# Kernel tuning notes

Measured on AMD Instinct MI355X. Metric: run time of the kernel, lower is better.

The kernel has to match this reference:

```python
import jax, jax.numpy as jnp
import numpy as np

B, P, T, R, A = 16384, 3, 2, 3, 3   # batch, n_players, teammates, rivals, action_dim
HID = [1024, 512]
ENC_OUT = 64
RIVAL_START = 9 * 9 + 12 * P       # 117, as in the torch module
NEG_SLOPE = 0.01                    # nn.LeakyReLU default


def _linpack(key, k, din, dout):
    # PyTorch nn.Linear default init: U(-1/sqrt(din), 1/sqrt(din))
    kw, kb = jax.random.split(key)
    bound = 1.0 / np.sqrt(din)
    W = jax.random.uniform(kw, (k, din, dout), jnp.float32, -bound, bound)
    b = jax.random.uniform(kb, (k, dout), jnp.float32, -bound, bound)
    return W, b


def setup_inputs() -> dict:
    key = jax.random.key(0)
    ks = jax.random.split(key, 16)
    obs = jax.random.normal(ks[0], (B, P, 144), jnp.float32)
    act = jax.random.normal(ks[1], (B, P, A), jnp.float32)
    # stacked per-segment encoder weights (grouped small GEMMs)
    Wp1, bp1 = _linpack(ks[2], 9, 2 + A, 32)
    Wp2, bp2 = _linpack(ks[3], 9, 32, ENC_OUT)
    Wt1, bt1 = _linpack(ks[4], T, 12, 32)
    Wt2, bt2 = _linpack(ks[5], T, 32, ENC_OUT)
    Wr1, br1 = _linpack(ks[6], R, 9, 32)
    Wr2, br2 = _linpack(ks[7], R, 32, ENC_OUT)
    # q head: [P*896] -> 1024 -> 512 -> P
    din = P * (9 + T + R) * ENC_OUT
    Wq1, bq1 = _linpack(ks[8], 1, din, HID[0]);  Wq1, bq1 = Wq1[0], bq1[0]
    Wq2, bq2 = _linpack(ks[9], 1, HID[0], HID[1]); Wq2, bq2 = Wq2[0], bq2[0]
    Wq3, bq3 = _linpack(ks[10], 1, HID[1], P);   Wq3, bq3 = Wq3[0], bq3[0]
    return dict(obs=obs, act=act,
                Wp1=Wp1, bp1=bp1, Wp2=Wp2, bp2=bp2,
                Wt1=Wt1, bt1=bt1, Wt2=Wt2, bt2=bt2,
                Wr1=Wr1, br1=br1, Wr2=Wr2, br2=br2,
                Wq1=Wq1, bq1=bq1, Wq2=Wq2, bq2=bq2, Wq3=Wq3, bq3=bq3)


def _enc2(x, W1, b1, W2, b2):
    # x: [B, P, K, din]; W1: [K, din, 32]; W2: [K, 32, 64] -> [B, P, K, 64]
    lrelu = lambda v: jax.nn.leaky_relu(v, NEG_SLOPE)
    h = lrelu(jnp.einsum('bpki,kio->bpko', x, W1) + b1)
    return lrelu(jnp.einsum('bpkh,kho->bpko', h, W2) + b2)


def reference(obs, act, Wp1, bp1, Wp2, bp2, Wt1, bt1, Wt2, bt2,
              Wr1, br1, Wr2, br2, Wq1, bq1, Wq2, bq2, Wq3, bq3):
    b = obs.shape[0]
    # prop segments: obs[:, :, 2i:2i+2] concat act  -> [B, P, 9, 2+A]
    x_prop = jnp.concatenate(
        [obs[:, :, :18].reshape(b, P, 9, 2),
         jnp.broadcast_to(act[:, :, None, :], (b, P, 9, A))], axis=-1)
    x_team = obs[:, :, 18:18 + 12 * T].reshape(b, P, T, 12)
    x_riv = obs[:, :, RIVAL_START:RIVAL_START + 9 * R].reshape(b, P, R, 9)
    ep = _enc2(x_prop, Wp1, bp1, Wp2, bp2)   # [B, P, 9, 64]
    et = _enc2(x_team, Wt1, bt1, Wt2, bt2)   # [B, P, T, 64]
    er = _enc2(x_riv, Wr1, br1, Wr2, br2)    # [B, P, R, 64]
    enc = jnp.concatenate([ep, et, er], axis=2).reshape(b, -1)  # [B, P*14*64]
    # q head: ReLU hidden activations, identity output
    h = jax.nn.relu(enc @ Wq1 + bq1)
    h = jax.nn.relu(h @ Wq2 + bq2)
    return h @ Wq3 + bq3                      # [B, P]
```

## Files before the change

kernel.cpp:

```cpp
#include <hip/hip_runtime.h>
#include <hip/hip_bf16.h>
#include <cstdint>

typedef __bf16 bf16x8 __attribute__((ext_vector_type(8)));
typedef float f32x4 __attribute__((ext_vector_type(4)));

__device__ __forceinline__ void gld16(const __bf16* g, __bf16* lds) {
    __builtin_amdgcn_global_load_lds(
        (__attribute__((address_space(1))) void*)(uintptr_t)g,
        (__attribute__((address_space(3))) void*)(uint32_t)(uintptr_t)lds,
        16, 0, 0);
}

__global__ __launch_bounds__(256) void prep_all(const float* __restrict__ Wq1, const float* __restrict__ Wq2,
                                                const float* __restrict__ Wp1, const float* __restrict__ bp1,
                                                const float* __restrict__ Wp2, const float* __restrict__ bp2,
                                                const float* __restrict__ Wt1, const float* __restrict__ bt1,
                                                const float* __restrict__ Wt2, const float* __restrict__ bt2,
                                                const float* __restrict__ Wr1, const float* __restrict__ br1,
                                                const float* __restrict__ Wr2, const float* __restrict__ br2,
                                                __bf16* __restrict__ w1t, __bf16* __restrict__ w2t,
                                                float* __restrict__ w1p, __bf16* __restrict__ w2e) {
    __shared__ float t[64][65];
    const int idx = blockIdx.x, tid = threadIdx.x;
    if (idx < 800) {
        const float* in; __bf16* out; int R, C, bx, by;
        if (idx < 672) { in = Wq1; out = w1t; R = 2688; C = 1024; bx = idx % 42; by = idx / 42; }
        else { const int i2 = idx - 672; in = Wq2; out = w2t; R = 1024; C = 512; bx = i2 % 16; by = i2 / 16; }
        const int r0 = bx * 64, c0 = by * 64;
#pragma unroll
        for (int i = 0; i < 16; i++) {
            int id2 = i * 256 + tid;
            int rr = id2 >> 6, cc = id2 & 63;
            t[rr][cc] = in[(size_t)(r0 + rr) * C + (c0 + cc)];
        }
        __syncthreads();
#pragma unroll
        for (int i = 0; i < 16; i++) {
            int id2 = i * 256 + tid;
            int rr = id2 >> 6, cc = id2 & 63;
            out[(size_t)(c0 + rr) * R + (r0 + cc)] = (__bf16)t[cc][rr];
        }
    } else {
        const int s = idx - 800;
        int ks, din, w1off;
        const float *W1, *B1, *W2, *B2;
        if (s < 9)      { ks = s;      din = 5;  w1off = s * 160;
                          W1 = Wp1; B1 = bp1; W2 = Wp2; B2 = bp2; }
        else if (s < 11){ ks = s - 9;  din = 12; w1off = 1440 + ks * 384;
                          W1 = Wt1; B1 = bt1; W2 = Wt2; B2 = bt2; }
        else            { ks = s - 11; din = 9;  w1off = 2208 + ks * 288;
                          W1 = Wr1; B1 = br1; W2 = Wr2; B2 = br2; }
        W1 += ks * din * 32; B1 += ks * 32; W2 += ks * 2048; B2 += ks * 64;
        for (int i = tid; i < din * 32; i += 256) w1p[w1off + i] = W1[i];
        if (tid < 32) w1p[3072 + s * 32 + tid] = B1[tid];
        if (tid < 64) w1p[3520 + s * 64 + tid] = B2[tid];
        for (int i = tid; i < 2048; i += 256) {
            const int o = i >> 5, k = i & 31;
            w2e[s * 2048 + i] = (__bf16)W2[k * 64 + o];
        }
    }
}

__global__ __launch_bounds__(256) void enc_fused(const float* __restrict__ obs,
                                                 const float* __restrict__ act,
                                                 const float* __restrict__ w1p,
                                                 const __bf16* __restrict__ w2t,
                                                 __bf16* __restrict__ enc) {
    __shared__ float sW[4416];
    __shared__ __bf16 sH[2][64 * 40];
    __shared__ __align__(16) __bf16 sO[2][64 * 72];
    const int tid = threadIdx.x;
    for (int i = tid; i < 4416; i += 256) sW[i] = w1p[i];
    const int rloc = tid >> 2, q = tid & 3;
    const int row = blockIdx.x * 64 + rloc;
    const float* orow = obs + (size_t)row * 144;
    const float a0 = act[row * 3], a1 = act[row * 3 + 1], a2 = act[row * 3 + 2];
    const int wv = tid >> 6, lane = tid & 63;
    const int fr = lane & 15, kq = lane >> 4;

    bf16x8 bfrA[4], bfrB[4];
    int curH = 0, curO = 0;

    auto prefetchB = [&](int sn) {
#pragma unroll
        for (int n = 0; n < 4; n++)
            bfrB[n] = *(const bf16x8*)&w2t[(sn * 64 + n * 16 + fr) * 32 + kq * 8];
    };
    auto storeOut = [&](int sp, int bO) {
#pragma unroll
        for (int h = 0; h < 2; h++) {
            const int c = tid + h * 256;
            const int r = c >> 3, ch = c & 7;
            const bf16x8 v = *(const bf16x8*)&sO[bO][r * 72 + ch * 8];
            *(bf16x8*)&enc[((size_t)blockIdx.x * 64 + r) * 896 + sp * 64 + ch * 8] = v;
        }
    };
    auto l2c = [&](int s, int bH, int bO) {
        const bf16x8 afr = *(const bf16x8*)&sH[bH][(wv * 16 + fr) * 40 + kq * 8];
        f32x4 acc[4] = {};
#pragma unroll
        for (int n = 0; n < 4; n++)
            acc[n] = __builtin_amdgcn_mfma_f32_16x16x32_bf16(afr, bfrA[n], acc[n], 0, 0, 0);
        const float* b2 = sW + 3520 + s * 64;
#pragma unroll
        for (int n = 0; n < 4; n++) {
            const float bv = b2[n * 16 + fr];
#pragma unroll
            for (int rg = 0; rg < 4; rg++) {
                float v = acc[n][rg] + bv;
                v = fmaxf(v, 0.01f * v);
                sO[bO][(wv * 16 + kq * 4 + rg) * 72 + n * 16 + fr] = (__bf16)v;
            }
        }
    };

#define L1(DIN, W1OFF, SGI, DH, XLOAD)                               \
    {                                                                \
        float x[DIN];                                                \
        XLOAD;                                                       \
        const float* w1 = sW + (W1OFF);                              \
        const float* b1 = sW + 3072 + (SGI) * 32;                    \
        bf16x8 t_;                                                   \
        _Pragma("unroll") for (int j = 0; j < 8; j++) {              \
            const int o = q * 8 + j;                                 \
            float a_ = b1[o];                                        \
            _Pragma("unroll") for (int i = 0; i < DIN; i++)          \
                a_ += x[i] * w1[i * 32 + o];                         \
            t_[j] = (__bf16)fmaxf(a_, 0.01f * a_);                   \
        }                                                            \
        *(bf16x8*)&sH[DH][rloc * 40 + q * 8] = t_;                   \
    }

#define PROPX(K) { x[0] = orow[2 * (K)]; x[1] = orow[2 * (K) + 1]; x[2] = a0; x[3] = a1; x[4] = a2; }
#define TEAMX(K) { _Pragma("unroll") for (int i = 0; i < 12; i++) x[i] = orow[18 + 12 * (K) + i]; }
#define RIVX(K)  { _Pragma("unroll") for (int i = 0; i < 9; i++) x[i] = orow[117 + 9 * (K) + i]; }

#define STEP(S, NEXTL1)                                              \
    __syncthreads();                                                 \
    if ((S) < 13) prefetchB((S) + 1);                                \
    if ((S) > 0) storeOut((S) - 1, curO ^ 1);                        \
    l2c((S), curH, curO);                                            \
    _Pragma("unroll") for (int n = 0; n < 4; n++) bfrA[n] = bfrB[n]; \
    NEXTL1                                                           \
    curH ^= 1; curO ^= 1;

    prefetchB(0);
    __syncthreads();
#pragma unroll
    for (int n = 0; n < 4; n++) bfrA[n] = bfrB[n];
    L1(5, 0, 0, 0, PROPX(0))

    STEP(0,  L1(5, 160, 1, curH ^ 1, PROPX(1)))
    STEP(1,  L1(5, 320, 2, curH ^ 1, PROPX(2)))
    STEP(2,  L1(5, 480, 3, curH ^ 1, PROPX(3)))
    STEP(3,  L1(5, 640, 4, curH ^ 1, PROPX(4)))
    STEP(4,  L1(5, 800, 5, curH ^ 1, PROPX(5)))
    STEP(5,  L1(5, 960, 6, curH ^ 1, PROPX(6)))
    STEP(6,  L1(5, 1120, 7, curH ^ 1, PROPX(7)))
    STEP(7,  L1(5, 1280, 8, curH ^ 1, PROPX(8)))
    STEP(8,  L1(12, 1440, 9, curH ^ 1, TEAMX(0)))
    STEP(9,  L1(12, 1824, 10, curH ^ 1, TEAMX(1)))
    STEP(10, L1(9, 2208, 11, curH ^ 1, RIVX(0)))
    STEP(11, L1(9, 2496, 12, curH ^ 1, RIVX(1)))
    STEP(12, L1(9, 2784, 13, curH ^ 1, RIVX(2)))
    STEP(13, )

    __syncthreads();
    storeOut(13, curO ^ 1);
#undef STEP
#undef L1
#undef PROPX
#undef TEAMX
#undef RIVX
}

template <int NB, bool HEAD>
__global__ __launch_bounds__(512, 2) void gemm256_relu(const __bf16* __restrict__ Ag,
                                                       const __bf16* __restrict__ Btg,
                                                       const float* __restrict__ bias,
                                                       __bf16* __restrict__ Cg,
                                                       const float* __restrict__ Wq3,
                                                       float* __restrict__ pout,
                                                       int N, int K, int lgn) {
    __shared__ __align__(16) __bf16 ldsF[32768 + 2 * 2 * NB * 4096];
    const int tid = threadIdx.x;
    const int wid = tid >> 6, lane = tid & 63;
    const int wm = wid >> 2, wn = wid & 3;
    const int fr = lane & 15, kq = lane >> 4;

    const int chunk = gridDim.x >> 3;
    const int wg = (blockIdx.x & 7) * chunk + (blockIdx.x >> 3);
    const int bn = wg & ((1 << lgn) - 1), bm = wg >> lgn;

    const int c0 = tid, c1 = tid + 512;
    const int r0 = c0 >> 3, s0 = (c0 & 7) ^ (r0 & 7);
    const int r1 = c1 >> 3, s1 = (c1 & 7) ^ (r1 & 7);
    const size_t aH = (size_t)128 * K;
    const size_t bH = (size_t)(NB * 64) * K;
    const __bf16* aB0 = Ag + (size_t)(bm * 256 + r0) * K + s0 * 8;
    const __bf16* aB1 = Ag + (size_t)(bm * 256 + r1) * K + s1 * 8;
    const __bf16* bB0 = Btg + (size_t)(bn * (NB * 128) + r0) * K + s0 * 8;
    const __bf16* bB1 = Btg + (size_t)(bn * (NB * 128) + r1) * K + s1 * 8;

    f32x4 acc[2][2][4][NB] = {};
    bf16x8 a0[4][2], a1[4][2], b0[NB][2], b1[NB][2];

#define LDSA(BUF, H) (ldsF + ((BUF) * 2 + (H)) * 8192)
#define LDSB(BUF, H) (ldsF + 32768 + ((BUF) * 2 + (H)) * (NB * 4096))

#define STAGE_A(BUF, H, KO)                                   \
    do {                                                      \
        __bf16* d_ = LDSA(BUF, H);                            \
        gld16(aB0 + (H)*aH + (KO), d_ + c0 * 8);              \
        gld16(aB1 + (H)*aH + (KO), d_ + c1 * 8);              \
    } while (0)
#define STAGE_B(BUF, H, KO)                                   \
    do {                                                      \
        __bf16* d_ = LDSB(BUF, H);                            \
        gld16(bB0 + (H)*bH + (KO), d_ + c0 * 8);              \
        if constexpr (NB == 2) gld16(bB1 + (H)*bH + (KO), d_ + c1 * 8); \
    } while (0)

#define LDFA(BUF, H, ROW, KS) \
    (*(const bf16x8*)&LDSA(BUF, H)[(ROW) * 64 + ((((KS)*4 + kq) ^ ((ROW)&7)) * 8)])
#define LDFB(BUF, H, ROW, KS) \
    (*(const bf16x8*)&LDSB(BUF, H)[(ROW) * 64 + ((((KS)*4 + kq) ^ ((ROW)&7)) * 8)])

#define LOAD_A(BUF, H, DST)                                   \
    _Pragma("unroll") for (int m = 0; m < 4; m++)             \
        _Pragma("unroll") for (int ks = 0; ks < 2; ks++)      \
            DST[m][ks] = LDFA(BUF, H, wm * 64 + m * 16 + fr, ks);
#define LOAD_B(BUF, H, DST)                                   \
    _Pragma("unroll") for (int n = 0; n < NB; n++)            \
        _Pragma("unroll") for (int ks = 0; ks < 2; ks++)      \
            DST[n][ks] = LDFB(BUF, H, wn * (NB * 16) + n * 16 + fr, ks);

#define MM(Q, R, AR, BR)                                      \
    __builtin_amdgcn_s_setprio(1);                            \
    _Pragma("unroll") for (int ks = 0; ks < 2; ks++)          \
        _Pragma("unroll") for (int m = 0; m < 4; m++)         \
            _Pragma("unroll") for (int n = 0; n < NB; n++)    \
                acc[Q][R][m][n] = __builtin_amdgcn_mfma_f32_16x16x32_bf16( \
                    AR[m][ks], BR[n][ks], acc[Q][R][m][n], 0, 0, 0); \
    __builtin_amdgcn_s_setprio(0);

#define SB0 __builtin_amdgcn_sched_barrier(0)
#define BAR __builtin_amdgcn_s_barrier()
#define LGKM_B1                                               \
    if constexpr (NB == 2) asm volatile("s_waitcnt lgkmcnt(4)" ::: "memory"); \
    else asm volatile("s_waitcnt lgkmcnt(2)" ::: "memory");
#define LGKM(NSTR) asm volatile("s_waitcnt lgkmcnt(" NSTR ")" ::: "memory")
#define VMW(NSTR) asm volatile("s_waitcnt vmcnt(" NSTR ")" ::: "memory")
#define VMW2(N2, N1)                                          \
    if constexpr (NB == 2) VMW(#N2); else VMW(#N1);

    const int NT = K >> 6;

    STAGE_A(0, 0, 0);
    STAGE_B(0, 0, 0);
    STAGE_B(0, 1, 0);
    STAGE_A(0, 1, 0);
    VMW("2");
    BAR;
    LOAD_A(0, 0, a0)
    LOAD_B(0, 0, b0)
    SB0;

    for (int t = 0; t < NT - 1; ++t) {
        const int buf = t & 1, nb = buf ^ 1;
        const int kO = (t + 1) << 6;

        STAGE_A(nb, 0, kO);
        STAGE_B(nb, 0, kO);
        VMW2(4, 3);
        LOAD_B(buf, 1, b1)
        SB0;
        BAR;
        LGKM_B1;
        SB0;
        MM(0, 0, a0, b0)

        STAGE_B(nb, 1, kO);
        STAGE_A(nb, 1, kO);
        LOAD_A(buf, 1, a1)
        SB0;
        BAR;
        LGKM("8");
        SB0;
        MM(0, 1, a0, b1)

        BAR;
        LGKM("0");
        SB0;
        MM(1, 0, a1, b0)

        VMW("2");
        BAR;
        LOAD_A(nb, 0, a0)
        LOAD_B(nb, 0, b0)
        SB0;
        MM(1, 1, a1, b1)
    }

    {
        const int buf = (NT - 1) & 1;
        VMW("0");
        LOAD_B(buf, 1, b1)
        SB0;
        BAR;
        LGKM_B1;
        SB0;
        MM(0, 0, a0, b0)

        LOAD_A(buf, 1, a1)
        SB0;
        BAR;
        LGKM("8");
        SB0;
        MM(0, 1, a0, b1)

        BAR;
        LGKM("0");
        SB0;
        MM(1, 0, a1, b0)

        MM(1, 1, a1, b1)
    }

    const int cc = lane & 15, rr = (lane >> 4) << 2;
    if constexpr (!HEAD) {
#pragma unroll
        for (int q = 0; q < 2; q++)
#pragma unroll
            for (int r2 = 0; r2 < 2; r2++)
#pragma unroll
                for (int m = 0; m < 4; m++)
#pragma unroll
                    for (int n = 0; n < NB; n++) {
                        const int colG = bn * (NB * 128) + r2 * (NB * 64) + wn * (NB * 16) + n * 16 + cc;
                        const int rowG = bm * 256 + q * 128 + wm * 64 + m * 16 + rr;
                        const float bv = bias[colG];
#pragma unroll
                        for (int reg = 0; reg < 4; reg++) {
                            float v = acc[q][r2][m][n][reg] + bv;
                            v = fmaxf(v, 0.0f);
                            Cg[(size_t)(rowG + reg) * N + colG] = (__bf16)v;
                        }
                    }
    } else {
        __syncthreads();
        __bf16* hS = ldsF;
#pragma unroll
        for (int q = 0; q < 2; q++)
#pragma unroll
            for (int r2 = 0; r2 < 2; r2++)
#pragma unroll
                for (int m = 0; m < 4; m++) {
                    const int colL = r2 * 64 + wn * 16 + cc;
                    const int rowL0 = q * 128 + wm * 64 + m * 16 + rr;
                    const float bv = bias[bn * 128 + colL];
                    const int slot = colL >> 3, pos = colL & 7;
#pragma unroll
                    for (int reg = 0; reg < 4; reg++) {
                        const int rowL = rowL0 + reg;
                        float v = acc[q][r2][m][0][reg] + bv;
                        v = fmaxf(v, 0.0f);
                        hS[rowL * 128 + (slot ^ (rowL & 7)) * 8 + pos] = (__bf16)v;
                    }
                }
        __syncthreads();
        const int rowL = tid >> 1, half = tid & 1;
        float s0 = 0.f, s1 = 0.f, s2 = 0.f;
#pragma unroll
        for (int c8 = 0; c8 < 8; c8++) {
            const int lslot = half * 8 + c8;
            const int pslot = half * 8 + (c8 ^ (rowL & 7));
            const bf16x8 hv = *(const bf16x8*)&hS[rowL * 128 + pslot * 8];
#pragma unroll
            for (int j = 0; j < 8; j++) {
                const float hf = (float)hv[j];
                const int col = bn * 128 + lslot * 8 + j;
                s0 += hf * Wq3[col * 3 + 0];
                s1 += hf * Wq3[col * 3 + 1];
                s2 += hf * Wq3[col * 3 + 2];
            }
        }
        s0 += __shfl_xor(s0, 1);
        s1 += __shfl_xor(s1, 1);
        s2 += __shfl_xor(s2, 1);
        if (!half) {
            float* p = pout + ((size_t)(bm * 256 + rowL) * 4 + bn) * 3;
            p[0] = s0; p[1] = s1; p[2] = s2;
        }
    }
#undef LDSA
#undef LDSB
#undef STAGE_A
#undef STAGE_B
#undef LDFA
#undef LDFB
#undef LOAD_A
#undef LOAD_B
#undef MM
#undef SB0
#undef BAR
#undef LGKM_B1
#undef LGKM
#undef VMW
#undef VMW2
}

__global__ __launch_bounds__(256) void reduce_head(const float* __restrict__ pout,
                                                   const float* __restrict__ bq3,
                                                   float* __restrict__ out) {
    const int row = blockIdx.x * 256 + threadIdx.x;
    const float* p = pout + (size_t)row * 12;
#pragma unroll
    for (int j = 0; j < 3; j++)
        out[(size_t)row * 3 + j] = p[j] + p[3 + j] + p[6 + j] + p[9 + j] + bq3[j];
}

extern "C" void kernel_launch(void* const* d_in, const int* in_sizes, int n_in,
                              void* d_out, int out_size, void* d_ws, size_t ws_size,
                              hipStream_t stream) {
    const float* obs = (const float*)d_in[0];
    const float* act = (const float*)d_in[1];
    const float* Wp1 = (const float*)d_in[2];  const float* bp1 = (const float*)d_in[3];
    const float* Wp2 = (const float*)d_in[4];  const float* bp2 = (const float*)d_in[5];
    const float* Wt1 = (const float*)d_in[6];  const float* bt1 = (const float*)d_in[7];
    const float* Wt2 = (const float*)d_in[8];  const float* bt2 = (const float*)d_in[9];
    const float* Wr1 = (const float*)d_in[10]; const float* br1 = (const float*)d_in[11];
    const float* Wr2 = (const float*)d_in[12]; const float* br2 = (const float*)d_in[13];
    const float* Wq1 = (const float*)d_in[14]; const float* bq1 = (const float*)d_in[15];
    const float* Wq2 = (const float*)d_in[16]; const float* bq2 = (const float*)d_in[17];
    const float* Wq3 = (const float*)d_in[18]; const float* bq3 = (const float*)d_in[19];
    float* out = (float*)d_out;

    char* ws = (char*)d_ws;
    __bf16* enc  = (__bf16*)(ws);
    __bf16* h1   = (__bf16*)(ws + 88080384);
    float*  pout = (float*)(ws + 88080384 + 33554432);
    __bf16* w1t  = (__bf16*)(ws + 138412032);
    __bf16* w2t  = (__bf16*)(ws + 143917056);
    float*  w1p  = (float*)(ws + 144965632);
    __bf16* w2e  = (__bf16*)(ws + 144983296);

    prep_all<<<814, 256, 0, stream>>>(Wq1, Wq2, Wp1, bp1, Wp2, bp2, Wt1, bt1, Wt2, bt2,
                                      Wr1, br1, Wr2, br2, w1t, w2t, w1p, w2e);

    enc_fused<<<768, 256, 0, stream>>>(obs, act, w1p, w2e, enc);

    gemm256_relu<2, false><<<dim3(256), 512, 0, stream>>>(enc, w1t, bq1, h1, nullptr, nullptr, 1024, 2688, 2);
    gemm256_relu<1, true><<<dim3(256), 512, 0, stream>>>(h1, w2t, bq2, nullptr, Wq3, pout, 512, 1024, 2);
    reduce_head<<<64, 256, 0, stream>>>(pout, bq3, out);
}
```

Before: 136.7 us.

## Simplify GEMM main loop to one barrier per K-tile with bulk prefetch

Replaces the finely interleaved double-buffered K loop, which had several barriers per iteration and a peeled final iteration, with a simpler loop. Each iteration waits for all outstanding global-to-LDS loads and syncs once. It then reads its fragments, issues all four staging loads for the next tile at once, and runs the four MFMA quadrants with only lgkmcnt waits between them. The aim is to cut barrier and wait overhead inside the hot loop. In exchange, global loads are no longer spread across the MFMA phases, and the full vmcnt(0) wait at the top of the loop may expose more memory latency.

After: 135.3 us. About the same (-1.0%).

```diff
diff --git a/kernel.cpp b/kernel.cpp
--- a/kernel.cpp
+++ b/kernel.cpp
@@ -247,13 +247,10 @@
 
 #define SB0 __builtin_amdgcn_sched_barrier(0)
 #define BAR __builtin_amdgcn_s_barrier()
-#define LGKM_B1                                               \
-    if constexpr (NB == 2) asm volatile("s_waitcnt lgkmcnt(4)" ::: "memory"); \
-    else asm volatile("s_waitcnt lgkmcnt(2)" ::: "memory");
 #define LGKM(NSTR) asm volatile("s_waitcnt lgkmcnt(" NSTR ")" ::: "memory")
+#define LGKM2(N2, N1)                                         \
+    if constexpr (NB == 2) LGKM(#N2); else LGKM(#N1);
 #define VMW(NSTR) asm volatile("s_waitcnt vmcnt(" NSTR ")" ::: "memory")
-#define VMW2(N2, N1)                                          \
-    if constexpr (NB == 2) VMW(#N2); else VMW(#N1);
 
     const int NT = K >> 6;
 
@@ -261,70 +258,35 @@
     STAGE_B(0, 0, 0);
     STAGE_B(0, 1, 0);
     STAGE_A(0, 1, 0);
-    VMW("2");
-    BAR;
-    LOAD_A(0, 0, a0)
-    LOAD_B(0, 0, b0)
-    SB0;
-
-    for (int t = 0; t < NT - 1; ++t) {
+
+    for (int t = 0; t < NT; ++t) {
         const int buf = t & 1, nb = buf ^ 1;
         const int kO = (t + 1) << 6;
 
-        STAGE_A(nb, 0, kO);
-        STAGE_B(nb, 0, kO);
-        VMW2(4, 3);
+        VMW("0");
+        BAR;
+        LOAD_A(buf, 0, a0)
+        LOAD_B(buf, 0, b0)
+        SB0;
+        if (t + 1 < NT) {
+            STAGE_A(nb, 0, kO);
+            STAGE_B(nb, 0, kO);
+            STAGE_B(nb, 1, kO);
+            STAGE_A(nb, 1, kO);
+        }
+        SB0;
         LOAD_B(buf, 1, b1)
-        SB0;
-        BAR;
-        LGKM_B1;
+        LOAD_A(buf, 1, a1)
+        SB0;
+        LGKM2(12, 10);
         SB0;
         MM(0, 0, a0, b0)
-
-        STAGE_B(nb, 1, kO);
-        STAGE_A(nb, 1, kO);
-        LOAD_A(buf, 1, a1)
-        SB0;
-        BAR;
         LGKM("8");
         SB0;
         MM(0, 1, a0, b1)
-
-        BAR;
         LGKM("0");
         SB0;
         MM(1, 0, a1, b0)
-
-        VMW("2");
-        BAR;
-        LOAD_A(nb, 0, a0)
-        LOAD_B(nb, 0, b0)
-        SB0;
-        MM(1, 1, a1, b1)
-    }
-
-    {
-        const int buf = (NT - 1) & 1;
-        VMW("0");
-        LOAD_B(buf, 1, b1)
-        SB0;
-        BAR;
-        LGKM_B1;
-        SB0;
-        MM(0, 0, a0, b0)
-
-        LOAD_A(buf, 1, a1)
-        SB0;
-        BAR;
-        LGKM("8");
-        SB0;
-        MM(0, 1, a0, b1)
-
-        BAR;
-        LGKM("0");
-        SB0;
-        MM(1, 0, a1, b0)
-
         MM(1, 1, a1, b1)
     }
 
@@ -405,10 +367,9 @@
 #undef MM
 #undef SB0
 #undef BAR
-#undef LGKM_B1
 #undef LGKM
+#undef LGKM2
 #undef VMW
-#undef VMW2
 }
 
 __global__ __launch_bounds__(256) void reduce_head(const float* __restrict__ pout,
```

## Add selectable GEMM pipeline schedules and use a simpler schedule for the head GEMM

Applied to the files above, without the earlier changes.

Adds a SCHED template parameter to the 256-tile GEMM. Schedule 0 folds the tail iteration into the main loop and issues the next tile's A/B fragment loads earlier, interleaved with the MFMA blocks. Schedule 1 uses one barrier per K-step, prefetches the whole next tile at once and waits on LDS counters between MFMA blocks. The first GEMM keeps schedule 0 and the smaller head GEMM uses schedule 1, which trades overlap for fewer barriers. Hand-written waitcnt values must match the number of outstanding loads, or the kernel reads stale data.

Result: no change. 138.2 us (+1.1%).

```diff
diff --git a/kernel.cpp b/kernel.cpp
--- a/kernel.cpp
+++ b/kernel.cpp
@@ -175,7 +175,7 @@
 #undef RIVX
 }
 
-template <int NB, bool HEAD>
+template <int NB, bool HEAD, int SCHED>
 __global__ __launch_bounds__(512, 2) void gemm256_relu(const __bf16* __restrict__ Ag,
                                                        const __bf16* __restrict__ Btg,
                                                        const float* __restrict__ bias,
@@ -247,85 +247,107 @@
 
 #define SB0 __builtin_amdgcn_sched_barrier(0)
 #define BAR __builtin_amdgcn_s_barrier()
-#define LGKM_B1                                               \
-    if constexpr (NB == 2) asm volatile("s_waitcnt lgkmcnt(4)" ::: "memory"); \
-    else asm volatile("s_waitcnt lgkmcnt(2)" ::: "memory");
 #define LGKM(NSTR) asm volatile("s_waitcnt lgkmcnt(" NSTR ")" ::: "memory")
+#define LGKM2(N2, N1)                                         \
+    if constexpr (NB == 2) LGKM(#N2); else LGKM(#N1);
 #define VMW(NSTR) asm volatile("s_waitcnt vmcnt(" NSTR ")" ::: "memory")
 #define VMW2(N2, N1)                                          \
     if constexpr (NB == 2) VMW(#N2); else VMW(#N1);
 
     const int NT = K >> 6;
 
-    STAGE_A(0, 0, 0);
-    STAGE_B(0, 0, 0);
-    STAGE_B(0, 1, 0);
-    STAGE_A(0, 1, 0);
-    VMW("2");
-    BAR;
-    LOAD_A(0, 0, a0)
-    LOAD_B(0, 0, b0)
-    SB0;
-
-    for (int t = 0; t < NT - 1; ++t) {
-        const int buf = t & 1, nb = buf ^ 1;
-        const int kO = (t + 1) << 6;
-
-        STAGE_A(nb, 0, kO);
-        STAGE_B(nb, 0, kO);
-        VMW2(4, 3);
-        LOAD_B(buf, 1, b1)
-        SB0;
-        BAR;
-        LGKM_B1;
-        SB0;
-        MM(0, 0, a0, b0)
-
-        STAGE_B(nb, 1, kO);
-        STAGE_A(nb, 1, kO);
-        LOAD_A(buf, 1, a1)
-        SB0;
-        BAR;
-        LGKM("8");
-        SB0;
-        MM(0, 1, a0, b1)
-
-        BAR;
-        LGKM("0");
-        SB0;
-        MM(1, 0, a1, b0)
-
+    if constexpr (SCHED == 0) {
+        STAGE_A(0, 0, 0);
+        STAGE_B(0, 0, 0);
+        STAGE_B(0, 1, 0);
+        STAGE_A(0, 1, 0);
         VMW("2");
         BAR;
-        LOAD_A(nb, 0, a0)
-        LOAD_B(nb, 0, b0)
+        LOAD_A(0, 0, a0)
+        LOAD_B(0, 0, b0)
         SB0;
-        MM(1, 1, a1, b1)
-    }
-
-    {
-        const int buf = (NT - 1) & 1;
-        VMW("0");
-        LOAD_B(buf, 1, b1)
-        SB0;
-        BAR;
-        LGKM_B1;
-        SB0;
-        MM(0, 0, a0, b0)
-
-        LOAD_A(buf, 1, a1)
-        SB0;
-        BAR;
-        LGKM("8");
-        SB0;
-        MM(0, 1, a0, b1)
-
-        BAR;
-        LGKM("0");
-        SB0;
-        MM(1, 0, a1, b0)
-
-        MM(1, 1, a1, b1)
+
+        for (int t = 0; t < NT; ++t) {
+            const int buf = t & 1, nb = buf ^ 1;
+            const int kO = (t + 1) << 6;
+            const bool st = (t + 1 < NT);
+
+            if (st) {
+                STAGE_A(nb, 0, kO);
+                STAGE_B(nb, 0, kO);
+                VMW2(4, 3);
+            } else {
+                VMW("0");
+            }
+            LOAD_B(buf, 1, b1)
+            SB0;
+            BAR;
+            LGKM2(4, 2);
+            SB0;
+            MM(0, 0, a0, b0)
+
+            if (st) {
+                STAGE_B(nb, 1, kO);
+                STAGE_A(nb, 1, kO);
+            }
+            LOAD_A(buf, 1, a1)
+            SB0;
+            if (st) VMW2(4, 3);
+            BAR;
+            LGKM("8");
+            SB0;
+            MM(0, 1, a0, b1)
+
+            BAR;
+            if (st) { LOAD_A(nb, 0, a0) }
+            SB0;
+            if (st) { LGKM("8"); }
+            else { LGKM("0"); }
+            SB0;
+            MM(1, 0, a1, b0)
+
+            if (st) VMW("2");
+            BAR;
+            if (st) { LOAD_B(nb, 0, b0) }
+            SB0;
+            MM(1, 1, a1, b1)
+        }
+    } else {
+        STAGE_A(0, 0, 0);
+        STAGE_B(0, 0, 0);
+        STAGE_B(0, 1, 0);
+        STAGE_A(0, 1, 0);
+
+        for (int t = 0; t < NT; ++t) {
+            const int buf = t & 1, nb = buf ^ 1;
+            const int kO = (t + 1) << 6;
+
+            VMW("0");
+            BAR;
+            LOAD_A(buf, 0, a0)
+            LOAD_B(buf, 0, b0)
+            SB0;
+            if (t + 1 < NT) {
+                STAGE_A(nb, 0, kO);
+                STAGE_B(nb, 0, kO);
+                STAGE_B(nb, 1, kO);
+                STAGE_A(nb, 1, kO);
+            }
+            SB0;
+            LOAD_B(buf, 1, b1)
+            LOAD_A(buf, 1, a1)
+            SB0;
+            LGKM2(12, 10);
+            SB0;
+            MM(0, 0, a0, b0)
+            LGKM("8");
+            SB0;
+            MM(0, 1, a0, b1)
+            LGKM("0");
+            SB0;
+            MM(1, 0, a1, b0)
+            MM(1, 1, a1, b1)
+        }
     }
 
     const int cc = lane & 15, rr = (lane >> 4) << 2;
@@ -371,7 +393,7 @@
                 }
         __syncthreads();
         const int rowL = tid >> 1, half = tid & 1;
-        float s0 = 0.f, s1 = 0.f, s2 = 0.f;
+        float s0v = 0.f, s1v = 0.f, s2v = 0.f;
 #pragma unroll
         for (int c8 = 0; c8 < 8; c8++) {
             const int lslot = half * 8 + c8;
@@ -381,17 +403,17 @@
             for (int j = 0; j < 8; j++) {
                 const float hf = (float)hv[j];
                 const int col = bn * 128 + lslot * 8 + j;
-                s0 += hf * Wq3[col * 3 + 0];
-                s1 += hf * Wq3[col * 3 + 1];
-                s2 += hf * Wq3[col * 3 + 2];
+                s0v += hf * Wq3[col * 3 + 0];
+                s1v += hf * Wq3[col * 3 + 1];
+                s2v += hf * Wq3[col * 3 + 2];
             }
         }
-        s0 += __shfl_xor(s0, 1);
-        s1 += __shfl_xor(s1, 1);
-        s2 += __shfl_xor(s2, 1);
+        s0v += __shfl_xor(s0v, 1);
+        s1v += __shfl_xor(s1v, 1);
+        s2v += __shfl_xor(s2v, 1);
         if (!half) {
             float* p = pout + ((size_t)(bm * 256 + rowL) * 4 + bn) * 3;
-            p[0] = s0; p[1] = s1; p[2] = s2;
+            p[0] = s0v; p[1] = s1v; p[2] = s2v;
         }
     }
 #undef LDSA
@@ -405,8 +427,8 @@
 #undef MM
 #undef SB0
 #undef BAR
-#undef LGKM_B1
 #undef LGKM
+#undef LGKM2
 #undef VMW
 #undef VMW2
 }
@@ -451,7 +473,7 @@
 
     enc_fused<<<768, 256, 0, stream>>>(obs, act, w1p, w2e, enc);
 
-    gemm256_relu<2, false><<<dim3(256), 512, 0, stream>>>(enc, w1t, bq1, h1, nullptr, nullptr, 1024, 2688, 2);
-    gemm256_relu<1, true><<<dim3(256), 512, 0, stream>>>(h1, w2t, bq2, nullptr, Wq3, pout, 512, 1024, 2);
+    gemm256_relu<2, false, 0><<<dim3(256), 512, 0, stream>>>(enc, w1t, bq1, h1, nullptr, nullptr, 1024, 2688, 2);
+    gemm256_relu<1, true, 1><<<dim3(256), 512, 0, stream>>>(h1, w2t, bq2, nullptr, Wq3, pout, 512, 1024, 2);
     reduce_head<<<64, 256, 0, stream>>>(pout, bq3, out);
 }
```
